# Optimization experiments

Hardware: AMD Instinct MI355X
Metric: run time of the kernel (lower is better)

Reference implementation:

```python
import jax, jax.numpy as jnp
import numpy as np

T_OUT = 12  # num_timesteps_output


def setup_inputs() -> dict:
    key = jax.random.key(0)
    ks = jax.random.split(key, 12)
    B, N, T, F = 32, 325, 12, 2
    C, H = 10, 64
    s = 0.08  # weight init scale (~1/sqrt(H)) to keep gates in sane range
    return {
        "A": jnp.zeros((N, N), jnp.float32),
        "X": jax.random.normal(ks[0], (B, N, T, F), jnp.float32),
        "enc_Wih": jax.random.normal(ks[1], (C, 3 * H, F), jnp.float32) * s,
        "enc_Whh": jax.random.normal(ks[2], (C, 3 * H, H), jnp.float32) * s,
        "enc_bih": jax.random.normal(ks[3], (C, 3 * H), jnp.float32) * s,
        "enc_bhh": jax.random.normal(ks[4], (C, 3 * H), jnp.float32) * s,
        "dec_Wih": jax.random.normal(ks[5], (C, 3 * H, 1), jnp.float32) * s,
        "dec_Whh": jax.random.normal(ks[6], (C, 3 * H, H), jnp.float32) * s,
        "dec_bih": jax.random.normal(ks[7], (C, 3 * H), jnp.float32) * s,
        "dec_bhh": jax.random.normal(ks[8], (C, 3 * H), jnp.float32) * s,
        "lin_W": jax.random.normal(ks[9], (C, 1, H), jnp.float32) * s,
        "lin_b": jax.random.normal(ks[10], (C, 1), jnp.float32) * s,
        "embed": jax.random.normal(ks[11], (N, C), jnp.float32),
    }


def _gru_update(gi, gh, h, H):
    # PyTorch GRU gate order: r, z, n
    r = jax.nn.sigmoid(gi[..., :H] + gh[..., :H])
    z = jax.nn.sigmoid(gi[..., H:2 * H] + gh[..., H:2 * H])
    n = jnp.tanh(gi[..., 2 * H:] + r * gh[..., 2 * H:])
    return (1.0 - z) * n + z * h


def reference(A, X, enc_Wih, enc_Whh, enc_bih, enc_bhh,
              dec_Wih, dec_Whh, dec_bih, dec_bhh, lin_W, lin_b, embed):
    B, N, T, F = X.shape
    C = enc_Wih.shape[0]
    H = enc_Whh.shape[-1]
    BN = B * N

    # (T, BN, F): time-major, batch*nodes flattened (matches X.view(-1,T,F).permute(1,0,2))
    Xs = jnp.transpose(X.reshape(BN, T, F), (1, 0, 2))

    def enc_step(h, x_t):  # h: (C, BN, H), x_t: (BN, F)
        gi = jnp.einsum('bf,cgf->cbg', x_t, enc_Wih) + enc_bih[:, None, :]
        gh = jnp.einsum('cbh,cgh->cbg', h, enc_Whh) + enc_bhh[:, None, :]
        return _gru_update(gi, gh, h, H), None

    h0 = jnp.zeros((C, BN, H), X.dtype)
    h_enc, _ = jax.lax.scan(enc_step, h0, Xs)  # (C, BN, H)

    # initial decoder input: last observed value of feature 0
    lv0 = jnp.broadcast_to(Xs[-1, :, 0][None, :, None], (C, BN, 1))

    def dec_step(carry, _):
        h, lv = carry
        gi = jnp.einsum('cbf,cgf->cbg', lv, dec_Wih) + dec_bih[:, None, :]
        gh = jnp.einsum('cbh,cgh->cbg', h, dec_Whh) + dec_bhh[:, None, :]
        h = _gru_update(gi, gh, h, H)
        value = jnp.einsum('cbh,coh->cbo', h, lin_W) + lin_b[:, None, :]  # (C, BN, 1)
        # original does last_value = value.detach()
        return (h, jax.lax.stop_gradient(value)), value

    (_, _), vals = jax.lax.scan(dec_step, (h_enc, lv0), None, length=T_OUT)
    # vals: (T_out, C, BN, 1) -> (B, N, T_out, C)
    out = jnp.transpose(vals[..., 0], (2, 0, 1)).reshape(B, N, T_OUT, C)

    weight = jax.nn.softmax(embed, axis=-1)  # (N, C)
    return jnp.einsum('bntc,nc->bnt', out, weight)
```

## Files before the change

### kernel.cpp

```cpp
#include <hip/hip_runtime.h>
#include <math.h>

#define N_     325
#define BN_    10400
#define OUTSZ_ (BN_*12)
#define RB_    208
#define WV_    13
#define THR_   832


typedef _Float16 h8v  __attribute__((ext_vector_type(8)));
typedef float    f4v  __attribute__((ext_vector_type(4)));
typedef unsigned int u32x4 __attribute__((ext_vector_type(4)));

#define L1C 1.4426950408889634f
#define L2C 2.8853900817779268f

__device__ __forceinline__ float rcp_f(float x){ return __builtin_amdgcn_rcpf(x); }
#if __has_builtin(__builtin_amdgcn_exp2f)
__device__ __forceinline__ float exp2_f(float x){ return __builtin_amdgcn_exp2f(x); }
#else
__device__ __forceinline__ float exp2_f(float x){ return __expf(x * 0.6931471805599453f); }
#endif

__device__ __forceinline__ unsigned short f16u(float x){
    union { _Float16 h; unsigned short u; } cv; cv.h = (_Float16)x; return cv.u;
}

#define BOFF   0
#define EOFF   24576
#define HOFF   27648
#define XOFF   57600
#define WOFF   67584
#define LOFF   68416
#define LWOFF  69248
#define SMEMSZ 71296

#define MFMA(A,B,C) __builtin_amdgcn_mfma_f32_16x16x32_f16((A),(B),(C),0,0,0)

__device__ __forceinline__ void stage_main(const float* __restrict__ W, char* smem, int tid)
{
#pragma unroll
    for (int it = 0; it < 2; ++it) {
        int a16 = it*THR_ + tid;
        if (a16 < 1536) {
            int f     = a16 >> 6;
            int lanew = a16 & 63;
            int colf  = lanew & 15;
            int kb4   = lanew >> 4;
            int ch    = f & 1;
            int ct    = (f >> 1) & 3;
            int g     = f >> 3;
            int gc    = g*64 + ct*16 + colf;
            int k0    = ch*32 + kb4*8;
            float sc  = (g < 2) ? -L1C : -L2C;
            const float* p = W + gc*64 + k0;
            float4 a = *(const float4*)p;
            float4 b = *(const float4*)(p+4);
            h8v v;
            v[0]=(_Float16)(sc*a.x); v[1]=(_Float16)(sc*a.y);
            v[2]=(_Float16)(sc*a.z); v[3]=(_Float16)(sc*a.w);
            v[4]=(_Float16)(sc*b.x); v[5]=(_Float16)(sc*b.y);
            v[6]=(_Float16)(sc*b.z); v[7]=(_Float16)(sc*b.w);
            *(h8v*)(smem + BOFF + a16*16) = v;
        }
    }
}

__device__ __forceinline__ void rnn_step(h8v Aeh, h8v Ah0, h8v Ah1,
                                         const char* bb, const char* eb,
                                         const float cbh[4], float (&hreg)[4][4],
                                         char* wp)
{
    const f4v Z0 = {0.f,0.f,0.f,0.f};
#pragma unroll
    for (int ct = 0; ct < 4; ++ct) {
        f4v a0 = MFMA(Aeh, *(const h8v*)(eb + ct*256),       Z0);
        a0 = MFMA(Ah0, *(const h8v*)(bb + (ct*2   )*1024), a0);
        a0 = MFMA(Ah1, *(const h8v*)(bb + (ct*2+1 )*1024), a0);
        f4v a1 = MFMA(Aeh, *(const h8v*)(eb + (4+ct)*256),   Z0);
        a1 = MFMA(Ah0, *(const h8v*)(bb + (8+ct*2 )*1024), a1);
        a1 = MFMA(Ah1, *(const h8v*)(bb + (9+ct*2 )*1024), a1);
        f4v a3 = MFMA(Aeh, *(const h8v*)(eb + (8+ct)*256),   Z0);
        f4v a2 = MFMA(Ah0, *(const h8v*)(bb + (16+ct*2)*1024), Z0);
        a2 = MFMA(Ah1, *(const h8v*)(bb + (17+ct*2)*1024), a2);
#pragma unroll
        for (int i = 0; i < 4; ++i) {
            float er = exp2_f(a0[i]);
            float rr = rcp_f(1.0f + er);
            float ez = exp2_f(a1[i]);
            float en = exp2_f(fmaf(rr, a2[i] + cbh[ct], a3[i]));
            float h  = hreg[ct][i];
            float aa = 1.0f + ez;
            float den = fmaf(en, aa, aa);
            float t1  = fmaf(-en, ez, ez);
            float t2  = fmaf(en, h, h);
            float hnew = (t1 + t2) * rcp_f(den);
            hreg[ct][i] = hnew;
            *(_Float16*)(wp + i*144 + 32*ct) = (_Float16)hnew;
        }
        __builtin_amdgcn_sched_barrier(0);
    }
}

__global__ void __launch_bounds__(THR_, 8) krnn_kernel(
    const float* __restrict__ X,
    const float* __restrict__ eWih, const float* __restrict__ eWhh,
    const float* __restrict__ ebih, const float* __restrict__ ebhh,
    const float* __restrict__ dWih, const float* __restrict__ dWhh,
    const float* __restrict__ dbih, const float* __restrict__ dbhh,
    const float* __restrict__ linW, const float* __restrict__ linb,
    const float* __restrict__ embed, float* __restrict__ ws)
{
    __shared__ __align__(16) char smem[SMEMSZ];

    const int c    = blockIdx.y;
    const int row0 = blockIdx.x * RB_;
    const int tid  = threadIdx.x;
    const int lane = tid & 63;
    const int w    = tid >> 6;
    const int l15  = lane & 15;
    const int kg   = lane >> 4;

    stage_main(eWhh + c*12288, smem, tid);

    if (tid < 192) {
        int e = tid >> 4, ln = tid & 15;
        int g = e >> 2, ct = e & 3;
        int gc = g*64 + ct*16 + ln;
        float sc = (g < 2) ? -L1C : -L2C;
        float w0 = eWih[c*384 + gc*2], w1 = eWih[c*384 + gc*2 + 1];
        float bb_ = (g < 2) ? (ebih[c*192+gc] + ebhh[c*192+gc]) : ebih[c*192+gc];
        unsigned short* d = (unsigned short*)(smem + EOFF + e*256 + ln*16);
        d[0] = f16u(sc*w0); d[1] = f16u(sc*w1); d[2] = f16u(sc*bb_);
        d[3]=0; d[4]=0; d[5]=0; d[6]=0; d[7]=0;
    }
    for (int i = tid; i < RB_*12; i += THR_) {
        int r = i / 12, t = i - r*12;
        int rg = row0 + r;
        const float* p = X + (size_t)rg*24 + t*2;
        unsigned v = (unsigned)f16u(p[0]) | ((unsigned)f16u(p[1]) << 16);
        *(unsigned*)(smem + XOFF + r*48 + t*4) = v;
    }
    if (tid < RB_) {
        int r = row0 + tid;
        int n = r % N_;
        float e[10], mx = -1e30f;
#pragma unroll
        for (int cc=0; cc<10; ++cc){ e[cc]=embed[n*10+cc]; mx=fmaxf(mx,e[cc]); }
        float den = 0.0f;
#pragma unroll
        for (int cc=0; cc<10; ++cc) den += exp2_f((e[cc]-mx)*L1C);
        *(float*)(smem + WOFF + tid*4) = exp2_f((e[c]-mx)*L1C) * rcp_f(den);
    }
    for (int i = tid; i < WV_*576; i += THR_)
        *(unsigned*)(smem + HOFF + i*4) = 0u;

    float cbh[4];
#pragma unroll
    for (int ct=0; ct<4; ++ct) cbh[ct] = -L2C * ebhh[c*192 + 128 + l15 + 16*ct];

    __syncthreads();

    char* hp = smem + HOFF + w*2304;
    const int rdo = l15*144 + kg*16;
    char* wp = hp + kg*576 + l15*2;
    const char* bb = smem + lane*16;
    const char* eb = smem + EOFF + l15*16;

    float hreg[4][4];
#pragma unroll
    for (int ct=0; ct<4; ++ct)
#pragma unroll
        for (int i=0;i<4;++i) hreg[ct][i] = 0.0f;

    for (int t = 0; t < 12; ++t) {
        unsigned xd = *(const unsigned*)(smem + XOFF + (w*16 + l15)*48 + t*4);
        union { u32x4 u; h8v h; } ae;
        ae.u.x = (lane < 16) ? xd : 0u;
        ae.u.y = (lane < 16) ? 0x00003C00u : 0u;
        ae.u.z = 0u; ae.u.w = 0u;
        h8v Ah0 = *(const h8v*)(hp + rdo);
        h8v Ah1 = *(const h8v*)(hp + rdo + 64);
        rnn_step(ae.h, Ah0, Ah1, bb, eb, cbh, hreg, wp);
    }

    unsigned aew = (*(const unsigned*)(smem + XOFF + (w*16 + l15)*48 + 44) & 0xFFFFu)
                   | 0x3C000000u;

    __syncthreads();

    stage_main(dWhh + c*12288, smem, tid);
    if (tid < 192) {
        int e = tid >> 4, ln = tid & 15;
        int g = e >> 2, ct = e & 3;
        int gc = g*64 + ct*16 + ln;
        float k0, k1;
        if (g < 2) { k0 = -L1C*dWih[c*192+gc]; k1 = -L1C*(dbih[c*192+gc]+dbhh[c*192+gc]); }
        else       { k0 = -L2C*dWih[c*192+gc]; k1 = -L2C*dbih[c*192+gc]; }
        unsigned short* d = (unsigned short*)(smem + EOFF + e*256 + ln*16);
        d[0] = f16u(k0); d[1] = f16u(k1);
        d[2]=0; d[3]=0; d[4]=0; d[5]=0; d[6]=0; d[7]=0;
    }
    if (tid < 128) {
        int ch = tid >> 6, ln = tid & 63;
        int kb = ch*32 + (ln >> 4)*8;
        unsigned short* d = (unsigned short*)(smem + LWOFF + ch*1024 + ln*16);
#pragma unroll
        for (int j=0;j<8;++j) d[j] = f16u(linW[c*64 + kb + j]);
    }
#pragma unroll
    for (int ct=0; ct<4; ++ct) cbh[ct] = -L2C * dbhh[c*192 + 128 + l15 + 16*ct];
    const float lb = linb[c];
    float* __restrict__ wsc = ws + (size_t)c * OUTSZ_;

    __syncthreads();

    for (int s = 0; s < 12; ++s) {
        h8v Ah0 = *(const h8v*)(hp + rdo);
        h8v Ah1 = *(const h8v*)(hp + rdo + 64);
        if (s > 0) {
            const f4v Zv = {0.f,0.f,0.f,0.f};
            f4v av = MFMA(Ah0, *(const h8v*)(smem + LWOFF + lane*16), Zv);
            av = MFMA(Ah1, *(const h8v*)(smem + LWOFF + 1024 + lane*16), av);
            if (l15 == 0) {
#pragma unroll
                for (int i=0;i<4;++i) {
                    float lv = av[i] + lb;
                    *(float*)(smem + LOFF + w*64 + (kg*4+i)*4) = lv;
                    int r = row0 + w*16 + kg*4 + i;
                    float wg = *(const float*)(smem + WOFF + (w*16 + kg*4 + i)*4);
                    wsc[(size_t)r*12 + (s-1)] = wg*lv;
                }
            }
            float lvme = *(const float*)(smem + LOFF + w*64 + l15*4);
            aew = (unsigned)f16u(lvme) | 0x3C000000u;
        }
        union { u32x4 u; h8v h; } ae;
        ae.u.x = (lane < 16) ? aew : 0u;
        ae.u.y = 0u; ae.u.z = 0u; ae.u.w = 0u;
        rnn_step(ae.h, Ah0, Ah1, bb, eb, cbh, hreg, wp);
    }

    {
        h8v Ah0 = *(const h8v*)(hp + rdo);
        h8v Ah1 = *(const h8v*)(hp + rdo + 64);
        const f4v Zv = {0.f,0.f,0.f,0.f};
        f4v av = MFMA(Ah0, *(const h8v*)(smem + LWOFF + lane*16), Zv);
        av = MFMA(Ah1, *(const h8v*)(smem + LWOFF + 1024 + lane*16), av);
        if (l15 == 0) {
#pragma unroll
            for (int i=0;i<4;++i) {
                float lv = av[i] + lb;
                int r = row0 + w*16 + kg*4 + i;
                float wg = *(const float*)(smem + WOFF + (w*16 + kg*4 + i)*4);
                wsc[(size_t)r*12 + 11] = wg*lv;
            }
        }
    }
}

__global__ void __launch_bounds__(256) mix_kernel(const float* __restrict__ ws,
                                                  float* __restrict__ out)
{
    int i = blockIdx.x * 256 + threadIdx.x;
    if (i < OUTSZ_) {
        float s = 0.0f;
#pragma unroll
        for (int c = 0; c < 10; ++c) s += ws[(size_t)c * OUTSZ_ + i];
        out[i] = s;
    }
}

extern "C" void kernel_launch(void* const* d_in, const int* in_sizes, int n_in,
                              void* d_out, int out_size, void* d_ws, size_t ws_size,
                              hipStream_t stream) {
    const float* X    = (const float*)d_in[1];
    const float* eWih = (const float*)d_in[2];
    const float* eWhh = (const float*)d_in[3];
    const float* ebih = (const float*)d_in[4];
    const float* ebhh = (const float*)d_in[5];
    const float* dWih = (const float*)d_in[6];
    const float* dWhh = (const float*)d_in[7];
    const float* dbih = (const float*)d_in[8];
    const float* dbhh = (const float*)d_in[9];
    const float* linW = (const float*)d_in[10];
    const float* linb = (const float*)d_in[11];
    const float* emb  = (const float*)d_in[12];
    float* ws  = (float*)d_ws;
    float* out = (float*)d_out;

    dim3 grid(BN_ / RB_, 10);
    krnn_kernel<<<grid, dim3(THR_), 0, stream>>>(
        X, eWih, eWhh, ebih, ebhh, dWih, dWhh, dbih, dbhh, linW, linb, emb, ws);
    mix_kernel<<<(OUTSZ_ + 255) / 256, dim3(256), 0, stream>>>(ws, out);
}
```

Baseline: 228.1 us.

## Replace padded hidden-state LDS layout with XOR swizzle and shrink shared memory

```diff
diff --git a/kernel.cpp b/kernel.cpp
--- a/kernel.cpp
+++ b/kernel.cpp
@@ -30,11 +30,11 @@
 #define BOFF   0
 #define EOFF   24576
 #define HOFF   27648
-#define XOFF   57600
-#define WOFF   67584
-#define LOFF   68416
-#define LWOFF  69248
-#define SMEMSZ 71296
+#define XOFF   54272
+#define LWOFF  54272
+#define LOFF   54400
+#define WOFF   64256
+#define SMEMSZ 65088
 
 #define MFMA(A,B,C) __builtin_amdgcn_mfma_f32_16x16x32_f16((A),(B),(C),0,0,0)
 
@@ -70,7 +70,7 @@
 __device__ __forceinline__ void rnn_step(h8v Aeh, h8v Ah0, h8v Ah1,
                                          const char* bb, const char* eb,
                                          const float cbh[4], float (&hreg)[4][4],
-                                         char* wp)
+                                         char* wb)
 {
     const f4v Z0 = {0.f,0.f,0.f,0.f};
 #pragma unroll
@@ -97,7 +97,7 @@
             float t2  = fmaf(en, h, h);
             float hnew = (t1 + t2) * rcp_f(den);
             hreg[ct][i] = hnew;
-            *(_Float16*)(wp + i*144 + 32*ct) = (_Float16)hnew;
+            *(_Float16*)(wb + i*128 + ((ct^i)<<5)) = (_Float16)hnew;
         }
         __builtin_amdgcn_sched_barrier(0);
     }
@@ -153,7 +153,7 @@
         for (int cc=0; cc<10; ++cc) den += exp2_f((e[cc]-mx)*L1C);
         *(float*)(smem + WOFF + tid*4) = exp2_f((e[c]-mx)*L1C) * rcp_f(den);
     }
-    for (int i = tid; i < WV_*576; i += THR_)
+    for (int i = tid; i < WV_*512; i += THR_)
         *(unsigned*)(smem + HOFF + i*4) = 0u;
 
     float cbh[4];
@@ -162,9 +162,10 @@
 
     __syncthreads();
 
-    char* hp = smem + HOFF + w*2304;
-    const int rdo = l15*144 + kg*16;
-    char* wp = hp + kg*576 + l15*2;
+    char* hp = smem + HOFF + w*2048;
+    const int rdo0 = l15*128 + ((((kg>>1) ^ (l15&3))<<5) | ((kg&1)<<4));
+    const int rdo1 = rdo0 ^ 64;
+    char* wb = hp + kg*512 + l15*2;
     const char* bb = smem + lane*16;
     const char* eb = smem + EOFF + l15*16;
 
@@ -180,9 +181,9 @@
         ae.u.x = (lane < 16) ? xd : 0u;
         ae.u.y = (lane < 16) ? 0x00003C00u : 0u;
         ae.u.z = 0u; ae.u.w = 0u;
-        h8v Ah0 = *(const h8v*)(hp + rdo);
-        h8v Ah1 = *(const h8v*)(hp + rdo + 64);
-        rnn_step(ae.h, Ah0, Ah1, bb, eb, cbh, hreg, wp);
+        h8v Ah0 = *(const h8v*)(hp + rdo0);
+        h8v Ah1 = *(const h8v*)(hp + rdo1);
+        rnn_step(ae.h, Ah0, Ah1, bb, eb, cbh, hreg, wb);
     }
 
     unsigned aew = (*(const unsigned*)(smem + XOFF + (w*16 + l15)*48 + 44) & 0xFFFFu)
@@ -202,12 +203,11 @@
         d[0] = f16u(k0); d[1] = f16u(k1);
         d[2]=0; d[3]=0; d[4]=0; d[5]=0; d[6]=0; d[7]=0;
     }
-    if (tid < 128) {
-        int ch = tid >> 6, ln = tid & 63;
-        int kb = ch*32 + (ln >> 4)*8;
-        unsigned short* d = (unsigned short*)(smem + LWOFF + ch*1024 + ln*16);
-#pragma unroll
-        for (int j=0;j<8;++j) d[j] = f16u(linW[c*64 + kb + j]);
+    if (tid < 8) {
+        int ch = tid >> 2, k4 = tid & 3;
+        unsigned short* d = (unsigned short*)(smem + LWOFF + ch*64 + k4*16);
+#pragma unroll
+        for (int j=0;j<8;++j) d[j] = f16u(linW[c*64 + ch*32 + k4*8 + j]);
     }
 #pragma unroll
     for (int ct=0; ct<4; ++ct) cbh[ct] = -L2C * dbhh[c*192 + 128 + l15 + 16*ct];
@@ -217,12 +217,12 @@
     __syncthreads();
 
     for (int s = 0; s < 12; ++s) {
-        h8v Ah0 = *(const h8v*)(hp + rdo);
-        h8v Ah1 = *(const h8v*)(hp + rdo + 64);
+        h8v Ah0 = *(const h8v*)(hp + rdo0);
+        h8v Ah1 = *(const h8v*)(hp + rdo1);
         if (s > 0) {
             const f4v Zv = {0.f,0.f,0.f,0.f};
-            f4v av = MFMA(Ah0, *(const h8v*)(smem + LWOFF + lane*16), Zv);
-            av = MFMA(Ah1, *(const h8v*)(smem + LWOFF + 1024 + lane*16), av);
+            f4v av = MFMA(Ah0, *(const h8v*)(smem + LWOFF + kg*16), Zv);
+            av = MFMA(Ah1, *(const h8v*)(smem + LWOFF + 64 + kg*16), av);
             if (l15 == 0) {
 #pragma unroll
                 for (int i=0;i<4;++i) {
@@ -239,15 +239,15 @@
         union { u32x4 u; h8v h; } ae;
         ae.u.x = (lane < 16) ? aew : 0u;
         ae.u.y = 0u; ae.u.z = 0u; ae.u.w = 0u;
-        rnn_step(ae.h, Ah0, Ah1, bb, eb, cbh, hreg, wp);
+        rnn_step(ae.h, Ah0, Ah1, bb, eb, cbh, hreg, wb);
     }
 
     {
-        h8v Ah0 = *(const h8v*)(hp + rdo);
-        h8v Ah1 = *(const h8v*)(hp + rdo + 64);
+        h8v Ah0 = *(const h8v*)(hp + rdo0);
+        h8v Ah1 = *(const h8v*)(hp + rdo1);
         const f4v Zv = {0.f,0.f,0.f,0.f};
-        f4v av = MFMA(Ah0, *(const h8v*)(smem + LWOFF + lane*16), Zv);
-        av = MFMA(Ah1, *(const h8v*)(smem + LWOFF + 1024 + lane*16), av);
+        f4v av = MFMA(Ah0, *(const h8v*)(smem + LWOFF + kg*16), Zv);
+        av = MFMA(Ah1, *(const h8v*)(smem + LWOFF + 64 + kg*16), av);
         if (l15 == 0) {
 #pragma unroll
             for (int i=0;i<4;++i) {
```

Result: no change. 228.8 us (+0.3%).
